# Kernel optimization log

Hardware: AMD Instinct MI355X
Metric: run time of the kernel (lower is better)

## Reference

```python
import jax, jax.numpy as jnp
import numpy as np

DIM = 1024
T = 16384
WINDOW = 32
DIM_HEAD = 64
HEADS = DIM // DIM_HEAD  # 16
EPS = 1e-5


def setup_inputs() -> dict:
    key = jax.random.key(0)
    k1, k2, k3 = jax.random.split(key, 3)
    x = jax.random.normal(k1, (DIM, T), dtype=jnp.float32)
    w_qkv = jax.random.normal(k2, (3 * DIM, DIM), dtype=jnp.float32) / np.float32(np.sqrt(DIM))
    w_out = jax.random.normal(k3, (DIM, DIM), dtype=jnp.float32) / np.float32(np.sqrt(DIM))
    gamma = jnp.ones((DIM,), dtype=jnp.float32)
    beta = jnp.zeros((DIM,), dtype=jnp.float32)
    return {"x": x, "w_qkv": w_qkv, "w_out": w_out, "gamma": gamma, "beta": beta}


def _rotate_half(t):
    # original: split channels into (2, d/2), swap halves with negation
    d = t.shape[-1]
    return jnp.concatenate((-t[..., d // 2:], t[..., :d // 2]), axis=-1)


def reference(x, w_qkv, w_out, gamma, beta):
    C, Tn = x.shape
    xt = x.T  # (T, C)
    # LayerNorm over channel dim (eqx.nn.LayerNorm, eps=1e-5)
    mu = jnp.mean(xt, axis=-1, keepdims=True)
    var = jnp.var(xt, axis=-1, keepdims=True)
    normed = (xt - mu) * jax.lax.rsqrt(var + EPS) * gamma + beta
    # QKV projection (Linear with weight (out,in), no bias)
    qkv = normed @ w_qkv.T  # (T, 3C)
    q, k, v = jnp.split(qkv, 3, axis=-1)
    w = Tn // WINDOW
    def towin(t):  # (w n) (h d) -> h w n d
        return t.reshape(w, WINDOW, HEADS, DIM_HEAD).transpose(2, 0, 1, 3)
    q, k, v = map(towin, (q, k, v))
    # rotary pos emb over window positions (use_xpos=False -> scale == 1)
    inv_freq = 1.0 / (10000.0 ** (jnp.arange(0, DIM_HEAD, 2, dtype=jnp.float32) / DIM_HEAD))
    tpos = jnp.arange(WINDOW, dtype=jnp.float32)
    freqs = jnp.einsum('i,j->ij', tpos, inv_freq)  # (n, d/2)
    freqs = jnp.concatenate((freqs, freqs), axis=-1)  # (n, d)
    cos, sin = jnp.cos(freqs), jnp.sin(freqs)
    q = q * cos + _rotate_half(q) * sin
    k = k * cos + _rotate_half(k) * sin
    # per-head, per-window full (non-causal) attention
    scale = DIM_HEAD ** -0.5
    logits = jnp.einsum('hwnd,hwmd->hwnm', q, k) * scale
    attn = jax.nn.softmax(logits, axis=-1)
    out = jnp.einsum('hwnm,hwmd->hwnd', attn, v)
    out = out.transpose(1, 2, 0, 3).reshape(Tn, C)  # h w n d -> (w n) (h d)
    out = out @ w_out.T
    return out.T + x
```

## Files before the change

kernel.cpp:

```cpp
#include <hip/hip_runtime.h>

#define T_TOK 16384
#define C_DIM 1024

typedef float f32x4 __attribute__((ext_vector_type(4)));
typedef float f32x16 __attribute__((ext_vector_type(16)));
typedef __bf16 bf16x8 __attribute__((ext_vector_type(8)));
typedef unsigned short u16x8 __attribute__((ext_vector_type(8)));
typedef unsigned short u16x4 __attribute__((ext_vector_type(4)));

__device__ __forceinline__ unsigned short f2bf(float f) {
  union { float f; unsigned u; } v; v.f = f;
  unsigned r = v.u + 0x7fffu + ((v.u >> 16) & 1u);
  return (unsigned short)(r >> 16);
}
__device__ __forceinline__ float bf2f(unsigned short h) {
  union { unsigned u; float f; } v; v.u = ((unsigned)h) << 16;
  return v.f;
}
__device__ __forceinline__ unsigned pk2(float a, float b) {
  return (unsigned)f2bf(a) | ((unsigned)f2bf(b) << 16);
}

__global__ __launch_bounds__(256) void cvt_kernel(const float* __restrict__ in,
                                                  unsigned short* __restrict__ out, int n4) {
  int i = blockIdx.x * 256 + threadIdx.x;
  if (i >= n4) return;
  f32x4 v = *(const f32x4*)(in + (size_t)i * 4);
  u16x4 o;
#pragma unroll
  for (int j = 0; j < 4; ++j) o[j] = f2bf(v[j]);
  *(u16x4*)(out + (size_t)i * 4) = o;
}

__global__ __launch_bounds__(256) void rope_tab_kernel(float* __restrict__ tab) {
  int idx = blockIdx.x * 256 + threadIdx.x;
  if (idx >= 1024) return;
  int mm = idx >> 5, d = idx & 31;
  float invf = powf(10000.f, -(float)d * (1.f / 32.f));
  float ang = (float)mm * invf;
  float s, c;
  sincosf(ang, &s, &c);
  tab[idx * 2] = c;
  tab[idx * 2 + 1] = s;
}

__global__ __launch_bounds__(256) void ln_stats_kernel(const float* __restrict__ x,
                                                       float* __restrict__ mu,
                                                       float* __restrict__ rstd) {
  __shared__ float s1[4][64];
  __shared__ float s2[4][64];
  const int tid = threadIdx.x;
  const int lt = tid & 63, cq = tid >> 6;
  const int t = blockIdx.x * 64 + lt;
  float s = 0.f, ss = 0.f;
  const float* p = x + (size_t)cq * 256 * T_TOK + t;
  for (int c = 0; c < 256; ++c) {
    float v = p[(size_t)c * T_TOK];
    s += v; ss += v * v;
  }
  s1[cq][lt] = s; s2[cq][lt] = ss;
  __syncthreads();
  if (tid < 64) {
    float S  = s1[0][tid] + s1[1][tid] + s1[2][tid] + s1[3][tid];
    float SS = s2[0][tid] + s2[1][tid] + s2[2][tid] + s2[3][tid];
    float m = S * (1.f / 1024.f);
    float var = SS * (1.f / 1024.f) - m * m;
    mu[blockIdx.x * 64 + tid] = m;
    rstd[blockIdx.x * 64 + tid] = rsqrtf(var + 1e-5f);
  }
}

__global__ __launch_bounds__(256) void ln_tr_kernel(const float* __restrict__ x,
                                                    const float* __restrict__ mu,
                                                    const float* __restrict__ rstd,
                                                    const float* __restrict__ gamma,
                                                    const float* __restrict__ beta,
                                                    unsigned short* __restrict__ normed) {
  __shared__ float tile[64][65];
  __shared__ float gs[64], bs[64], ms[64], rs[64];
  const int tid = threadIdx.x;
  const int bt = blockIdx.x & 255;
  const int bc = blockIdx.x >> 8;
  const int t0 = bt * 64, c0 = bc * 64;
  if (tid < 64) {
    gs[tid] = gamma[c0 + tid];
    bs[tid] = beta[c0 + tid];
    ms[tid] = mu[t0 + tid];
    rs[tid] = rstd[t0 + tid];
  }
  const int lc = tid >> 4;
  const int lt4 = (tid & 15) * 4;
#pragma unroll
  for (int r = 0; r < 4; ++r) {
    int c = r * 16 + lc;
    f32x4 v = *(const f32x4*)&x[(size_t)(c0 + c) * T_TOK + t0 + lt4];
    tile[c][lt4 + 0] = v[0]; tile[c][lt4 + 1] = v[1];
    tile[c][lt4 + 2] = v[2]; tile[c][lt4 + 3] = v[3];
  }
  __syncthreads();
#pragma unroll
  for (int r = 0; r < 2; ++r) {
    int idx = r * 256 + tid;
    int t = idx >> 3;
    int c8 = (idx & 7) * 8;
    float m = ms[t], rr = rs[t];
    u16x8 o;
#pragma unroll
    for (int j = 0; j < 8; ++j) {
      float v = tile[c8 + j][t];
      v = (v - m) * rr * gs[c8 + j] + bs[c8 + j];
      o[j] = f2bf(v);
    }
    *(u16x8*)&normed[(size_t)(t0 + t) * C_DIM + c0 + c8] = o;
  }
}

#define GLDS(gp, lp) \
  __builtin_amdgcn_global_load_lds((const __attribute__((address_space(1))) void*)(gp), \
                                   (__attribute__((address_space(3))) void*)(lp), 16, 0, 0)

#define BAR() __builtin_amdgcn_s_barrier()
#define LGKM0() asm volatile("s_waitcnt lgkmcnt(0)" ::: "memory")

template <int EPI>
__global__ __launch_bounds__(512, 2) void gemm8p_kernel(const unsigned short* __restrict__ A,
                                                        const unsigned short* __restrict__ B,
                                                        unsigned short* __restrict__ Obf,
                                                        int ldo, int nbn, int K,
                                                        const float* __restrict__ Xadd,
                                                        float* __restrict__ Ofp) {
  __shared__ unsigned short Lds[2][2][2][8192];
  const int tid = threadIdx.x;
  const int w = tid >> 6, lane = tid & 63;
  const int wm = w >> 2, wn = w & 3;

  const int nbm = gridDim.x / nbn;
  const int mtpx = nbm >> 3;
  const int xcd = blockIdx.x & 7;
  const int ib = blockIdx.x >> 3;
  const int mt = xcd * mtpx + (ib % mtpx);
  const int nt = ib / mtpx;
  const size_t m0 = (size_t)mt * 256, n0 = (size_t)nt * 256;

  const unsigned short* gA = A + (m0 + (lane >> 3)) * (size_t)K + ((lane & 7) ^ (lane >> 3)) * 8;
  const unsigned short* gB = B + (n0 + (lane >> 3)) * (size_t)K + ((lane & 7) ^ (lane >> 3)) * 8;
  const int wrow = w * 8;

  auto stageA = [&](int b, int h, int kt) {
    const unsigned short* g = gA + (size_t)(h * 128) * K + (size_t)kt * 64;
    GLDS(g + (size_t)wrow * K,        &Lds[0][b][h][wrow * 64]);
    GLDS(g + (size_t)(64 + wrow) * K, &Lds[0][b][h][(64 + wrow) * 64]);
  };
  auto stageB = [&](int b, int h, int kt) {
    const unsigned short* g = gB + (size_t)(h * 128) * K + (size_t)kt * 64;
    GLDS(g + (size_t)wrow * K,        &Lds[1][b][h][wrow * 64]);
    GLDS(g + (size_t)(64 + wrow) * K, &Lds[1][b][h][(64 + wrow) * 64]);
  };

  f32x4 acc[8][4];
#pragma unroll
  for (int i = 0; i < 8; ++i)
#pragma unroll
    for (int j = 0; j < 4; ++j) acc[i][j] = (f32x4){0.f, 0.f, 0.f, 0.f};

  const int KT = K >> 6;
  const int off_r = (lane & 15) * 64;
  const int slot0 = (((lane >> 4) ^ (lane & 7)) * 8);
  const int slot1 = slot0 ^ 32;
  const int boff = (wn & 1) * 4096;

  stageA(0, 0, 0); stageA(0, 1, 0); stageB(0, 0, 0); stageB(0, 1, 0);
  if (KT > 1) stageA(1, 0, 1);
  asm volatile("s_waitcnt vmcnt(2)" ::: "memory");
  BAR();

  int bb = 0;
  for (int t = 0; t < KT; ++t, bb ^= 1) {
    const unsigned short* Ab = &Lds[0][bb][wm][0];
    const unsigned short* Bb = &Lds[1][bb][wn >> 1][boff];
    bf16x8 aLo[4][2], aHi[4][2], bLo[2][2], bHi[2][2];

#pragma unroll
    for (int mi = 0; mi < 4; ++mi) {
      aLo[mi][0] = *(const bf16x8*)&Ab[mi * 1024 + off_r + slot0];
      aLo[mi][1] = *(const bf16x8*)&Ab[mi * 1024 + off_r + slot1];
    }
#pragma unroll
    for (int ni = 0; ni < 2; ++ni) {
      bLo[ni][0] = *(const bf16x8*)&Bb[ni * 1024 + off_r + slot0];
      bLo[ni][1] = *(const bf16x8*)&Bb[ni * 1024 + off_r + slot1];
    }
    if (t + 1 < KT) stageA(bb ^ 1, 1, t + 1);
    BAR();
    LGKM0();
    __builtin_amdgcn_s_setprio(1);
#pragma unroll
    for (int mi = 0; mi < 4; ++mi)
#pragma unroll
      for (int ni = 0; ni < 2; ++ni)
#pragma unroll
        for (int ks = 0; ks < 2; ++ks)
          acc[mi][ni] = __builtin_amdgcn_mfma_f32_16x16x32_bf16(aLo[mi][ks], bLo[ni][ks], acc[mi][ni], 0, 0, 0);
    __builtin_amdgcn_s_setprio(0);
    BAR();

#pragma unroll
    for (int ni = 0; ni < 2; ++ni) {
      bHi[ni][0] = *(const bf16x8*)&Bb[(ni + 2) * 1024 + off_r + slot0];
      bHi[ni][1] = *(const bf16x8*)&Bb[(ni + 2) * 1024 + off_r + slot1];
    }
    if (t + 1 < KT) stageB(bb ^ 1, 0, t + 1);
    BAR();
    LGKM0();
    __builtin_amdgcn_s_setprio(1);
#pragma unroll
    for (int mi = 0; mi < 4; ++mi)
#pragma unroll
      for (int ni = 0; ni < 2; ++ni)
#pragma unroll
        for (int ks = 0; ks < 2; ++ks)
          acc[mi][ni + 2] = __builtin_amdgcn_mfma_f32_16x16x32_bf16(aLo[mi][ks], bHi[ni][ks], acc[mi][ni + 2], 0, 0, 0);
    __builtin_amdgcn_s_setprio(0);
    BAR();

#pragma unroll
    for (int mi = 0; mi < 4; ++mi) {
      aHi[mi][0] = *(const bf16x8*)&Ab[(mi + 4) * 1024 + off_r + slot0];
      aHi[mi][1] = *(const bf16x8*)&Ab[(mi + 4) * 1024 + off_r + slot1];
    }
    if (t + 1 < KT) stageB(bb ^ 1, 1, t + 1);
    BAR();
    LGKM0();
    __builtin_amdgcn_s_setprio(1);
#pragma unroll
    for (int mi = 0; mi < 4; ++mi)
#pragma unroll
      for (int ni = 0; ni < 2; ++ni)
#pragma unroll
        for (int ks = 0; ks < 2; ++ks)
          acc[mi + 4][ni + 2] = __builtin_amdgcn_mfma_f32_16x16x32_bf16(aHi[mi][ks], bHi[ni][ks], acc[mi + 4][ni + 2], 0, 0, 0);
    __builtin_amdgcn_s_setprio(0);
    BAR();

    if (t + 2 < KT) {
      stageA(bb, 0, t + 2);
      asm volatile("s_waitcnt vmcnt(2)" ::: "memory");
    } else {
      asm volatile("s_waitcnt vmcnt(0)" ::: "memory");
    }
    BAR();
    __builtin_amdgcn_s_setprio(1);
#pragma unroll
    for (int mi = 0; mi < 4; ++mi)
#pragma unroll
      for (int ni = 0; ni < 2; ++ni)
#pragma unroll
        for (int ks = 0; ks < 2; ++ks)
          acc[mi + 4][ni] = __builtin_amdgcn_mfma_f32_16x16x32_bf16(aHi[mi][ks], bLo[ni][ks], acc[mi + 4][ni], 0, 0, 0);
    __builtin_amdgcn_s_setprio(0);
    BAR();
  }

  if (EPI == 0) {
    unsigned short* cw = &Lds[0][0][0][0] + (size_t)w * 8192;
#pragma unroll
    for (int mi = 0; mi < 8; ++mi)
#pragma unroll
      for (int ni = 0; ni < 4; ++ni)
#pragma unroll
        for (int r = 0; r < 4; ++r)
          cw[(mi * 16 + (lane >> 4) * 4 + r) * 64 + ni * 16 + (lane & 15)] = f2bf(acc[mi][ni][r]);
    LGKM0();
    const size_t gr0 = m0 + wm * 128;
    const size_t gc0 = n0 + wn * 64;
#pragma unroll
    for (int it = 0; it < 16; ++it) {
      int idx = it * 64 + lane;
      int rr = idx >> 3, c8 = (idx & 7) * 8;
      *(u16x8*)&Obf[(gr0 + rr) * (size_t)ldo + gc0 + c8] = *(const u16x8*)&cw[rr * 64 + c8];
    }
  } else {
    const size_t gr0 = m0 + wm * 128 + (lane >> 4) * 4;
    const size_t gc0 = n0 + wn * 64 + (lane & 15);
#pragma unroll
    for (int mi = 0; mi < 8; ++mi) {
      size_t row = gr0 + mi * 16;
#pragma unroll
      for (int ni = 0; ni < 4; ++ni) {
        size_t col = gc0 + ni * 16;
        f32x4 xv = *(const f32x4*)&Xadd[col * T_TOK + row];
        f32x4 o = acc[mi][ni] + xv;
        *(f32x4*)&Ofp[col * T_TOK + row] = o;
      }
    }
  }
}

__global__ __launch_bounds__(256) void attn_kernel(const unsigned short* __restrict__ qkv,
                                                   const float* __restrict__ ropeT,
                                                   unsigned short* __restrict__ aout) {
  __shared__ unsigned short Vt[4][64][32];
  const int tid = threadIdx.x;
  const int wv = tid >> 6;
  const int lane = tid & 63;
  const int m = lane & 31;
  const int hi = lane >> 5;
  const int gw = blockIdx.x * 4 + wv;
  const int w = gw >> 4, h = gw & 15;
  const size_t rowbase = ((size_t)(w * 32 + m)) * 3072 + (size_t)h * 64;
  const unsigned short* qp = qkv + rowbase;

  u16x8 qv[4], kv[4], vv[4];
#pragma unroll
  for (int s = 0; s < 4; ++s) {
    int off = s * 16 + hi * 8;
    qv[s] = *(const u16x8*)(qp + off);
    kv[s] = *(const u16x8*)(qp + 1024 + off);
    vv[s] = *(const u16x8*)(qp + 2048 + off);
  }

#pragma unroll
  for (int s = 0; s < 4; ++s)
#pragma unroll
    for (int j = 0; j < 8; ++j) {
      int d = s * 16 + hi * 8 + j;
      int slot = (((m >> 3) ^ (d ^ (d >> 2))) & 3) * 8 + (m & 7);
      Vt[wv][d][slot] = vv[s][j];
    }

  f32x4 ct[2][4];
  const float* tp = ropeT + (size_t)(m * 32 + hi * 8) * 2;
#pragma unroll
  for (int kp = 0; kp < 2; ++kp)
#pragma unroll
    for (int q = 0; q < 4; ++q)
      ct[kp][q] = *(const f32x4*)(tp + kp * 32 + q * 4);

  union FU { unsigned u[4]; bf16x8 v; };
  bf16x8 qfr[4], kfr[4];
#pragma unroll
  for (int ks = 0; ks < 4; ++ks) {
    const int kp = ks & 1;
    FU fq, fk;
#pragma unroll
    for (int jp = 0; jp < 4; ++jp) {
      float c0 = ct[kp][jp][0], s0 = ct[kp][jp][1];
      float c1 = ct[kp][jp][2], s1 = ct[kp][jp][3];
      float q0 = bf2f(qv[ks][2 * jp]), q1 = bf2f(qv[ks][2 * jp + 1]);
      float k0 = bf2f(kv[ks][2 * jp]), k1 = bf2f(kv[ks][2 * jp + 1]);
      float rq0, rq1, rk0, rk1;
      if (ks < 2) {
        rq0 = -bf2f(qv[ks + 2][2 * jp]); rq1 = -bf2f(qv[ks + 2][2 * jp + 1]);
        rk0 = -bf2f(kv[ks + 2][2 * jp]); rk1 = -bf2f(kv[ks + 2][2 * jp + 1]);
      } else {
        rq0 = bf2f(qv[ks - 2][2 * jp]); rq1 = bf2f(qv[ks - 2][2 * jp + 1]);
        rk0 = bf2f(kv[ks - 2][2 * jp]); rk1 = bf2f(kv[ks - 2][2 * jp + 1]);
      }
      fq.u[jp] = pk2(q0 * c0 + rq0 * s0, q1 * c1 + rq1 * s1);
      fk.u[jp] = pk2(k0 * c0 + rk0 * s0, k1 * c1 + rk1 * s1);
    }
    qfr[ks] = fq.v; kfr[ks] = fk.v;
  }

  f32x16 accS;
#pragma unroll
  for (int i = 0; i < 16; ++i) accS[i] = 0.f;
#pragma unroll
  for (int ks = 0; ks < 4; ++ks)
    accS = __builtin_amdgcn_mfma_f32_32x32x16_bf16(kfr[ks], qfr[ks], accS, 0, 0, 0);

  float p[16];
  float mx = -1e30f;
#pragma unroll
  for (int r = 0; r < 16; ++r) { p[r] = accS[r] * 0.125f; mx = fmaxf(mx, p[r]); }
  mx = fmaxf(mx, __shfl_xor(mx, 32, 64));
  float sum = 0.f;
#pragma unroll
  for (int r = 0; r < 16; ++r) { p[r] = __expf(p[r] - mx); sum += p[r]; }
  sum += __shfl_xor(sum, 32, 64);
  const float inv = 1.f / sum;
#pragma unroll
  for (int r = 0; r < 16; ++r) p[r] *= inv;

  bf16x8 pfr[2];
  {
    FU f0, f1;
    unsigned a0 = hi ? pk2(p[0], p[1]) : pk2(p[4], p[5]);
    unsigned a1 = hi ? pk2(p[2], p[3]) : pk2(p[6], p[7]);
    unsigned b0 = (unsigned)__shfl_xor((int)a0, 32, 64);
    unsigned b1 = (unsigned)__shfl_xor((int)a1, 32, 64);
    if (hi) { f0.u[0] = b0; f0.u[1] = b1; f0.u[2] = pk2(p[4], p[5]); f0.u[3] = pk2(p[6], p[7]); }
    else    { f0.u[0] = pk2(p[0], p[1]); f0.u[1] = pk2(p[2], p[3]); f0.u[2] = b0; f0.u[3] = b1; }
    unsigned a2 = hi ? pk2(p[8], p[9])   : pk2(p[12], p[13]);
    unsigned a3 = hi ? pk2(p[10], p[11]) : pk2(p[14], p[15]);
    unsigned b2 = (unsigned)__shfl_xor((int)a2, 32, 64);
    unsigned b3 = (unsigned)__shfl_xor((int)a3, 32, 64);
    if (hi) { f1.u[0] = b2; f1.u[1] = b3; f1.u[2] = pk2(p[12], p[13]); f1.u[3] = pk2(p[14], p[15]); }
    else    { f1.u[0] = pk2(p[8], p[9]); f1.u[1] = pk2(p[10], p[11]); f1.u[2] = b2; f1.u[3] = b3; }
    pfr[0] = f0.v; pfr[1] = f1.v;
  }

  f32x16 accO[2];
#pragma unroll
  for (int i = 0; i < 16; ++i) { accO[0][i] = 0.f; accO[1][i] = 0.f; }
  const int dl = lane & 31;
#pragma unroll
  for (int dh = 0; dh < 2; ++dh) {
    int d = dh * 32 + dl;
    int sx = (d ^ (d >> 2)) & 3;
#pragma unroll
    for (int ks = 0; ks < 2; ++ks) {
      bf16x8 vf = *(const bf16x8*)&Vt[wv][d][(((2 * ks + hi) ^ sx) & 3) * 8];
      accO[dh] = __builtin_amdgcn_mfma_f32_32x32x16_bf16(pfr[ks], vf, accO[dh], 0, 0, 0);
    }
  }

#pragma unroll
  for (int r = 0; r < 16; ++r) {
    int n = (r & 3) + 8 * (r >> 2) + 4 * hi;
    size_t o = (size_t)(w * 32 + n) * 1024 + h * 64 + dl;
    aout[o] = f2bf(accO[0][r]);
    aout[o + 32] = f2bf(accO[1][r]);
  }
}

extern "C" void kernel_launch(void* const* d_in, const int* in_sizes, int n_in,
                              void* d_out, int out_size, void* d_ws, size_t ws_size,
                              hipStream_t stream) {
  const float* x     = (const float*)d_in[0];
  const float* w_qkv = (const float*)d_in[1];
  const float* w_out = (const float*)d_in[2];
  const float* gamma = (const float*)d_in[3];
  const float* beta  = (const float*)d_in[4];

  char* ws = (char*)d_ws;
  unsigned short* wqkv_bf = (unsigned short*)(ws);
  unsigned short* wout_bf = (unsigned short*)(ws + 6291456);
  float* mu    = (float*)(ws + 8388608);
  float* rstd  = (float*)(ws + 8454144);
  float* ropeT = (float*)(ws + 8519680);
  unsigned short* normed = (unsigned short*)(ws + 8527872);
  unsigned short* qkv    = (unsigned short*)(ws + 42082304);
  unsigned short* aout   = normed;

  cvt_kernel<<<3072, 256, 0, stream>>>(w_qkv, wqkv_bf, 3072 * 1024 / 4);
  cvt_kernel<<<1024, 256, 0, stream>>>(w_out, wout_bf, 1024 * 1024 / 4);
  rope_tab_kernel<<<4, 256, 0, stream>>>(ropeT);
  ln_stats_kernel<<<256, 256, 0, stream>>>(x, mu, rstd);
  ln_tr_kernel<<<4096, 256, 0, stream>>>(x, mu, rstd, gamma, beta, normed);
  gemm8p_kernel<0><<<768, 512, 0, stream>>>(normed, wqkv_bf, qkv, 3072, 12, 1024,
                                            nullptr, nullptr);
  attn_kernel<<<2048, 256, 0, stream>>>(qkv, ropeT, aout);
  gemm8p_kernel<1><<<256, 512, 0, stream>>>(aout, wout_bf, nullptr, 0, 4, 1024,
                                            x, (float*)d_out);
}
```

Baseline: 220.4 us.

## Restructure GEMM main loop to prefetch a full tile ahead with fewer barriers

Reorganises the bf16 MFMA GEMM's software pipeline so that global-to-LDS staging runs two K-tiles ahead, issued as whole A/B tiles. LDS fragment reads for the next sub-block are issued before the current MFMA group rather than behind a barrier. The next tile's aLo/bLo fragments are loaded at the end of each iteration, and several intermediate barriers are removed. The aim is to hide LDS and global latency behind MFMA work. The cost is more outstanding loads and more live registers, plus a risk of LDS read/write races from the fewer barriers.

```diff
diff --git a/kernel.cpp b/kernel.cpp
--- a/kernel.cpp
+++ b/kernel.cpp
@@ -170,30 +170,42 @@
   const int slot1 = slot0 ^ 32;
   const int boff = (wn & 1) * 4096;
 
+  bf16x8 aLo[4][2], aHi[4][2], bLo[2][2], bHi[2][2];
+
   stageA(0, 0, 0); stageA(0, 1, 0); stageB(0, 0, 0); stageB(0, 1, 0);
-  if (KT > 1) stageA(1, 0, 1);
-  asm volatile("s_waitcnt vmcnt(2)" ::: "memory");
+  if (KT > 1) {
+    stageB(1, 0, 1); stageB(1, 1, 1); stageA(1, 0, 1); stageA(1, 1, 1);
+    asm volatile("s_waitcnt vmcnt(8)" ::: "memory");
+  } else {
+    asm volatile("s_waitcnt vmcnt(0)" ::: "memory");
+  }
   BAR();
+  {
+    const unsigned short* Ab = &Lds[0][0][wm][0];
+    const unsigned short* Bb = &Lds[1][0][wn >> 1][boff];
+#pragma unroll
+    for (int mi = 0; mi < 4; ++mi) {
+      aLo[mi][0] = *(const bf16x8*)&Ab[mi * 1024 + off_r + slot0];
+      aLo[mi][1] = *(const bf16x8*)&Ab[mi * 1024 + off_r + slot1];
+    }
+#pragma unroll
+    for (int ni = 0; ni < 2; ++ni) {
+      bLo[ni][0] = *(const bf16x8*)&Bb[ni * 1024 + off_r + slot0];
+      bLo[ni][1] = *(const bf16x8*)&Bb[ni * 1024 + off_r + slot1];
+    }
+  }
 
   int bb = 0;
   for (int t = 0; t < KT; ++t, bb ^= 1) {
     const unsigned short* Ab = &Lds[0][bb][wm][0];
     const unsigned short* Bb = &Lds[1][bb][wn >> 1][boff];
-    bf16x8 aLo[4][2], aHi[4][2], bLo[2][2], bHi[2][2];
-
-#pragma unroll
-    for (int mi = 0; mi < 4; ++mi) {
-      aLo[mi][0] = *(const bf16x8*)&Ab[mi * 1024 + off_r + slot0];
-      aLo[mi][1] = *(const bf16x8*)&Ab[mi * 1024 + off_r + slot1];
-    }
+
+    LGKM0();
 #pragma unroll
     for (int ni = 0; ni < 2; ++ni) {
-      bLo[ni][0] = *(const bf16x8*)&Bb[ni * 1024 + off_r + slot0];
-      bLo[ni][1] = *(const bf16x8*)&Bb[ni * 1024 + off_r + slot1];
-    }
-    if (t + 1 < KT) stageA(bb ^ 1, 1, t + 1);
-    BAR();
-    LGKM0();
+      bHi[ni][0] = *(const bf16x8*)&Bb[(ni + 2) * 1024 + off_r + slot0];
+      bHi[ni][1] = *(const bf16x8*)&Bb[(ni + 2) * 1024 + off_r + slot1];
+    }
     __builtin_amdgcn_s_setprio(1);
 #pragma unroll
     for (int mi = 0; mi < 4; ++mi)
@@ -205,14 +217,12 @@
     __builtin_amdgcn_s_setprio(0);
     BAR();
 
-#pragma unroll
-    for (int ni = 0; ni < 2; ++ni) {
-      bHi[ni][0] = *(const bf16x8*)&Bb[(ni + 2) * 1024 + off_r + slot0];
-      bHi[ni][1] = *(const bf16x8*)&Bb[(ni + 2) * 1024 + off_r + slot1];
-    }
-    if (t + 1 < KT) stageB(bb ^ 1, 0, t + 1);
-    BAR();
     LGKM0();
+#pragma unroll
+    for (int mi = 0; mi < 4; ++mi) {
+      aHi[mi][0] = *(const bf16x8*)&Ab[(mi + 4) * 1024 + off_r + slot0];
+      aHi[mi][1] = *(const bf16x8*)&Ab[(mi + 4) * 1024 + off_r + slot1];
+    }
     __builtin_amdgcn_s_setprio(1);
 #pragma unroll
     for (int mi = 0; mi < 4; ++mi)
@@ -224,14 +234,8 @@
     __builtin_amdgcn_s_setprio(0);
     BAR();
 
-#pragma unroll
-    for (int mi = 0; mi < 4; ++mi) {
-      aHi[mi][0] = *(const bf16x8*)&Ab[(mi + 4) * 1024 + off_r + slot0];
-      aHi[mi][1] = *(const bf16x8*)&Ab[(mi + 4) * 1024 + off_r + slot1];
-    }
-    if (t + 1 < KT) stageB(bb ^ 1, 1, t + 1);
-    BAR();
     LGKM0();
+    if (t + 2 < KT) { stageB(bb, 0, t + 2); stageB(bb, 1, t + 2); }
     __builtin_amdgcn_s_setprio(1);
 #pragma unroll
     for (int mi = 0; mi < 4; ++mi)
@@ -243,13 +247,15 @@
     __builtin_amdgcn_s_setprio(0);
     BAR();
 
-    if (t + 2 < KT) {
-      stageA(bb, 0, t + 2);
-      asm volatile("s_waitcnt vmcnt(2)" ::: "memory");
-    } else {
-      asm volatile("s_waitcnt vmcnt(0)" ::: "memory");
-    }
-    BAR();
+    if (t + 2 < KT) { stageA(bb, 0, t + 2); stageA(bb, 1, t + 2); }
+    if (t + 1 < KT) {
+      if (t + 2 < KT) {
+        asm volatile("s_waitcnt vmcnt(8)" ::: "memory");
+      } else {
+        asm volatile("s_waitcnt vmcnt(0)" ::: "memory");
+      }
+      BAR();
+    }
     __builtin_amdgcn_s_setprio(1);
 #pragma unroll
     for (int mi = 0; mi < 4; ++mi)
@@ -259,7 +265,20 @@
         for (int ks = 0; ks < 2; ++ks)
           acc[mi + 4][ni] = __builtin_amdgcn_mfma_f32_16x16x32_bf16(aHi[mi][ks], bLo[ni][ks], acc[mi + 4][ni], 0, 0, 0);
     __builtin_amdgcn_s_setprio(0);
-    BAR();
+    if (t + 1 < KT) {
+      const unsigned short* Ab2 = &Lds[0][bb ^ 1][wm][0];
+      const unsigned short* Bb2 = &Lds[1][bb ^ 1][wn >> 1][boff];
+#pragma unroll
+      for (int mi = 0; mi < 4; ++mi) {
+        aLo[mi][0] = *(const bf16x8*)&Ab2[mi * 1024 + off_r + slot0];
+        aLo[mi][1] = *(const bf16x8*)&Ab2[mi * 1024 + off_r + slot1];
+      }
+#pragma unroll
+      for (int ni = 0; ni < 2; ++ni) {
+        bLo[ni][0] = *(const bf16x8*)&Bb2[ni * 1024 + off_r + slot0];
+        bLo[ni][1] = *(const bf16x8*)&Bb2[ni * 1024 + off_r + slot1];
+      }
+    }
   }
 
   if (EPI == 0) {
```

Result: no change. 218.8 us (-0.7%).
